# Kernel optimization log

Hardware: AMD Instinct MI355X
Metric: run time of the kernel (lower is better)

The kernel has to match this reference:

```python
import jax, jax.numpy as jnp
import numpy as np

HID = 10
IN_DIM = 256
B, H, W = 8, 96, 96


def _conv(x, w, b=None, pad=0):
    y = jax.lax.conv_general_dilated(x, w, (1, 1), [(pad, pad), (pad, pad)],
                                     dimension_numbers=('NCHW', 'OIHW', 'NCHW'))
    return y if b is None else y + b[None, :, None, None]


def _bn(x, g, b):
    # eval-mode InPlaceABN(Sync) with identity running stats -> per-channel affine
    return x * g[None, :, None, None] + b[None, :, None, None]


def _branch(x, w1, g1, b1, w2, g2, b2):
    # Conv3x3 -> BN -> ReLU -> Conv1x1 -> BN -> ReLU  (relation / comp_u / comp_l)
    y = jax.nn.relu(_bn(_conv(x, w1, pad=1), g1, b1))
    return jax.nn.relu(_bn(_conv(y, w2), g2, b2))


def _gru(x, h, gw, gb, cw, cg, cb):
    # ConvGRU with 1x1 kernels
    gates = _conv(jnp.concatenate([x, h], axis=1), gw, gb)
    r = jax.nn.sigmoid(gates[:, 0:1])
    u = jax.nn.sigmoid(gates[:, 1:2])
    cnm = jax.nn.relu(_bn(_conv(jnp.concatenate([x, r * h], axis=1), cw), cg, cb))
    return (1.0 - u) * h + u * cnm


def setup_inputs():
    key = jax.random.key(0)
    ks = iter(jax.random.split(key, 48))

    def nrm(shape, s=0.05):
        return jax.random.normal(next(ks), shape, jnp.float32) * s

    inp = {
        'f_nodes': jax.random.normal(next(ks), (2, B, HID, H, W), jnp.float32),
        'h_nodes': jax.random.normal(next(ks), (3, B, HID, H, W), jnp.float32),
        'p_nodes': jax.random.normal(next(ks), (7, B, HID, H, W), jnp.float32),
        'xh': jax.random.normal(next(ks), (B, IN_DIM, H, W), jnp.float32),
        'f_atts': jax.random.uniform(next(ks), (2, B, 1, H, W), jnp.float32),
        'p_atts': jax.random.uniform(next(ks), (7, B, 1, H, W), jnp.float32),
        # Decomposition.decomp_att: Conv3x3(257->256)+BN+ReLU, Conv1x1(256->2)+bias
        'da_w1': nrm((IN_DIM, IN_DIM + 1, 3, 3)),
        'da_g1': jnp.ones((IN_DIM,), jnp.float32),
        'da_b1': jnp.zeros((IN_DIM,), jnp.float32),
        'da_w2': nrm((2, IN_DIM, 1, 1)),
        'da_b2': jnp.zeros((2,), jnp.float32),
    }
    # relation (shared across children), comp_u, comp_l: Conv3x3(20->10)+BN+ReLU, Conv1x1(10->10)+BN+ReLU
    for p in ('rel', 'cu', 'cl'):
        inp[p + '_w1'] = nrm((HID, 2 * HID, 3, 3))
        inp[p + '_g1'] = jnp.ones((HID,), jnp.float32)
        inp[p + '_b1'] = jnp.zeros((HID,), jnp.float32)
        inp[p + '_w2'] = nrm((HID, HID, 1, 1))
        inp[p + '_g2'] = jnp.ones((HID,), jnp.float32)
        inp[p + '_b2'] = jnp.zeros((HID,), jnp.float32)
    # 3 ConvGRUs (cls_h), 1x1 kernels, stacked on leading dim
    inp['gru_gw'] = nrm((3, 2, 2 * HID, 1, 1))
    inp['gru_gb'] = jnp.zeros((3, 2), jnp.float32)
    inp['gru_cw'] = nrm((3, HID, 2 * HID, 1, 1))
    inp['gru_cg'] = jnp.ones((3, HID), jnp.float32)
    inp['gru_cb'] = jnp.zeros((3, HID), jnp.float32)
    return inp


def reference(f_nodes, h_nodes, p_nodes, xh, f_atts, p_atts,
              da_w1, da_g1, da_b1, da_w2, da_b2,
              rel_w1, rel_g1, rel_b1, rel_w2, rel_g2, rel_b2,
              cu_w1, cu_g1, cu_b1, cu_w2, cu_g2, cu_b2,
              cl_w1, cl_g1, cl_b1, cl_w2, cl_g2, cl_b2,
              gru_gw, gru_gb, gru_cw, gru_cg, gru_cb):
    parent, parent_att = f_nodes[1], f_atts[1]
    # Decomposition of full-body node into 2 half nodes
    dm = _conv(jnp.concatenate([parent_att, xh], axis=1), da_w1, pad=1)
    dm = jax.nn.relu(_bn(dm, da_g1, da_b1))
    dm = _conv(dm, da_w2, da_b2)  # [B, 2, H, W] decomposition map
    datt = jax.nn.softmax(dm, axis=1)
    decomp = [_branch(jnp.concatenate([parent * datt[:, i:i + 1] * parent_att,
                                       h_nodes[1 + i]], axis=1),
                      rel_w1, rel_g1, rel_b1, rel_w2, rel_g2, rel_b2)
              for i in range(2)]
    # node 0: background
    n0 = _gru(f_nodes[0] + p_nodes[0], h_nodes[0],
              gru_gw[0], gru_gb[0], gru_cw[0], gru_cg[0], gru_cb[0])
    # node 1: upper half = composition(upper parts 1-4) + decomposition
    up = jnp.sum(p_nodes[1:5], axis=0) * jnp.sum(p_atts[1:5], axis=0)
    comp_u = _branch(jnp.concatenate([h_nodes[1], up], axis=1),
                     cu_w1, cu_g1, cu_b1, cu_w2, cu_g2, cu_b2)
    n1 = _gru(comp_u + decomp[0], h_nodes[1],
              gru_gw[1], gru_gb[1], gru_cw[1], gru_cg[1], gru_cb[1])
    # node 2: lower half = composition(lower parts 5-6) + decomposition
    lo = jnp.sum(p_nodes[5:7], axis=0) * jnp.sum(p_atts[5:7], axis=0)
    comp_l = _branch(jnp.concatenate([h_nodes[2], lo], axis=1),
                     cl_w1, cl_g1, cl_b1, cl_w2, cl_g2, cl_b2)
    n2 = _gru(comp_l + decomp[1], h_nodes[2],
              gru_gw[2], gru_gb[2], gru_cw[2], gru_cg[2], gru_cb[2])
    return (jnp.stack([n0, n1, n2]), dm)
```

## Files before the change

kernel.cpp:

```cpp
#include <hip/hip_runtime.h>
#include <cstddef>
#include <cstdint>

constexpr int Bn    = 8;
constexpr int Hn    = 96;
constexpr int Wn    = 96;
constexpr int HWn   = Hn * Wn;
constexpr int BHWn  = Bn * HWn;
constexpr int B10HW = Bn * 10 * HWn;

using short8  = __attribute__((ext_vector_type(8))) short;
using ushort8 = __attribute__((ext_vector_type(8))) unsigned short;
using float4v = __attribute__((ext_vector_type(4))) float;

__device__ __forceinline__ unsigned short f2bf(float f) {
    unsigned u = __builtin_bit_cast(unsigned, f);
    u += 0x7FFFu + ((u >> 16) & 1u);
    return (unsigned short)(u >> 16);
}

__global__ void k_packw(const float* __restrict__ w1, short* __restrict__ wpk)
{
    const int o = blockIdx.x * 256 + threadIdx.x;
    if (o >= 663552) return;
    const int j    = o & 7;
    const int lane = (o >> 3) & 63;
    const int q    = (o >> 9) & 15;
    const int t    = o >> 13;
    const int co   = q * 16 + (lane & 15);
    const int ci   = (t / 9) * 32 + ((lane >> 4) & 3) * 8 + j;
    const int tap  = t % 9;
    const float f  = (ci < 257) ? w1[((size_t)co * 257 + ci) * 9 + tap] : 0.f;
    wpk[o] = (short)f2bf(f);
}

__global__ __launch_bounds__(256, 3)
void k_bigconv3(const float* __restrict__ xh, const float* __restrict__ patt,
                const short* __restrict__ wpk, const float* __restrict__ g1,
                const float* __restrict__ b1, const float* __restrict__ w2,
                const float* __restrict__ db2,
                float* __restrict__ dm_out, float* __restrict__ s01)
{
    __shared__ __align__(16) short xs[2][4][137][8];
    __shared__ float part[4][64][2];

    const int tid  = threadIdx.x;
    const int lane = tid & 63;
    const int wid  = tid >> 6;
    const int bx   = blockIdx.x;
    const int b    = bx & 7;
    const int r2   = bx >> 3;
    const int wseg = r2 % 3;
    const int hb   = r2 / 3;
    const int h0   = hb * 2, w0 = wseg * 32;
    const int am   = lane & 15;
    const int aq   = lane >> 4;

    float4v acc[4][4];
    #pragma unroll
    for (int i = 0; i < 4; ++i)
        #pragma unroll
        for (int j = 0; j < 4; ++j)
            acc[i][j] = float4v{0.f, 0.f, 0.f, 0.f};

    int arow[4], acol[4];
    #pragma unroll
    for (int mt = 0; mt < 4; ++mt) {
        const int m = mt * 16 + am;
        arow[mt] = m >> 5;
        acol[mt] = m & 31;
    }

    auto stageX = [&](int cb, int buf) {
        const int cig0 = cb * 32 + wid * 8;
        for (int pos = lane; pos < 136; pos += 64) {
            const int row = pos / 34, col = pos % 34;
            const int hh = h0 - 1 + row, ww = w0 - 1 + col;
            const bool inb = ((unsigned)hh < (unsigned)Hn) & ((unsigned)ww < (unsigned)Wn);
            const int off = hh * Wn + ww;
            ushort8 v;
            #pragma unroll
            for (int j = 0; j < 8; ++j) {
                const int ci = cig0 + j;
                float f = 0.f;
                if (inb && ci < 257)
                    f = (ci == 0) ? patt[b * HWn + off]
                                  : xh[((size_t)b * 256 + (ci - 1)) * HWn + off];
                v[j] = f2bf(f);
            }
            *(ushort8*)&xs[buf][wid][pos][0] = v;
        }
    };

    const short8* wp = (const short8*)wpk;
    const int qb = wid * 4;

    stageX(0, 0);
    short8 bfr[4], bnx[4];
    #pragma unroll
    for (int nt = 0; nt < 4; ++nt)
        bfr[nt] = wp[(size_t)(qb + nt) * 64 + lane];
    __syncthreads();

    for (int cb = 0; cb < 9; ++cb) {
        const int buf = cb & 1;
        for (int tap = 0; tap < 9; ++tap) {
            const int t = cb * 9 + tap;
            if (t < 80) {
                #pragma unroll
                for (int nt = 0; nt < 4; ++nt)
                    bnx[nt] = wp[((size_t)(t + 1) * 16 + qb + nt) * 64 + lane];
            }
            const int kh = tap / 3, kw = tap % 3;
            short8 afr[4];
            #pragma unroll
            for (int mt = 0; mt < 4; ++mt) {
                const int pos = (arow[mt] + kh) * 34 + (acol[mt] + kw);
                afr[mt] = *(const short8*)&xs[buf][aq][pos][0];
            }
            #pragma unroll
            for (int mt = 0; mt < 4; ++mt)
                #pragma unroll
                for (int nt = 0; nt < 4; ++nt)
                    acc[mt][nt] = __builtin_amdgcn_mfma_f32_16x16x32_bf16(
                        afr[mt], bfr[nt], acc[mt][nt], 0, 0, 0);
            #pragma unroll
            for (int nt = 0; nt < 4; ++nt) bfr[nt] = bnx[nt];
        }
        if (cb < 8) stageX(cb + 1, buf ^ 1);
        __syncthreads();
    }

    float gv[4], bv[4], wa[4], wbv[4];
    #pragma unroll
    for (int nt = 0; nt < 4; ++nt) {
        const int co = wid * 64 + nt * 16 + am;
        gv[nt]  = g1[co];
        bv[nt]  = b1[co];
        wa[nt]  = w2[co];
        wbv[nt] = w2[256 + co];
    }
    #pragma unroll
    for (int mt = 0; mt < 4; ++mt) {
        #pragma unroll
        for (int reg = 0; reg < 4; ++reg) {
            float s0 = 0.f, s1 = 0.f;
            #pragma unroll
            for (int nt = 0; nt < 4; ++nt) {
                const float y = fmaxf(fmaf(acc[mt][nt][reg], gv[nt], bv[nt]), 0.f);
                s0 = fmaf(wa[nt], y, s0);
                s1 = fmaf(wbv[nt], y, s1);
            }
            #pragma unroll
            for (int off = 1; off < 16; off <<= 1) {
                s0 += __shfl_xor(s0, off, 64);
                s1 += __shfl_xor(s1, off, 64);
            }
            if (am == 0) {
                const int m = mt * 16 + aq * 4 + reg;
                part[wid][m][0] = s0;
                part[wid][m][1] = s1;
            }
        }
    }
    __syncthreads();
    if (tid < 64) {
        const int m = tid, r = m >> 5, c = m & 31;
        const int off = (h0 + r) * Wn + (w0 + c);
        float d0 = part[0][m][0] + part[1][m][0] + part[2][m][0] + part[3][m][0] + db2[0];
        float d1 = part[0][m][1] + part[1][m][1] + part[2][m][1] + part[3][m][1] + db2[1];
        dm_out[(size_t)(b * 2) * HWn + off]     = d0;
        dm_out[(size_t)(b * 2 + 1) * HWn + off] = d1;
        const float mx = fmaxf(d0, d1);
        const float e0 = expf(d0 - mx), e1 = expf(d1 - mx);
        const float pa = patt[b * HWn + off];
        const float inv = pa / (e0 + e1);
        s01[b * HWn + off]        = e0 * inv;
        s01[BHWn + b * HWn + off] = e1 * inv;
    }
}

struct BranchW  { const float *w1, *g1, *b1, *w2, *g2, *b2; };
struct BranchW3 { BranchW p[3]; };

__global__ __launch_bounds__(256)
void k_branch(BranchW3 P, const float* __restrict__ parent, const float* __restrict__ h_nodes,
              const float* __restrict__ s01, const float* __restrict__ pn,
              const float* __restrict__ pa, float* __restrict__ bout)
{
    const int z  = blockIdx.y;
    const int pi = (z < 2) ? 0 : (z - 1);
    __shared__ float xt[20][10][34];
    __shared__ float paSum[340];
    __shared__ __align__(16) float wlt[9 * 20 * 12];
    __shared__ float w2l[100], g1l[10], b1l[10], g2l[10], b2l[10];

    const BranchW& Pw = P.p[pi];
    const int tid = threadIdx.x;
    for (int idx = tid; idx < 2160; idx += 256) {
        const int co = idx % 12, rem = idx / 12, ci = rem % 20, tap = rem / 20;
        wlt[idx] = (co < 10) ? Pw.w1[(co * 20 + ci) * 9 + tap] : 0.f;
    }
    if (tid < 100) w2l[tid] = Pw.w2[tid];
    if (tid < 10) {
        g1l[tid] = Pw.g1[tid]; b1l[tid] = Pw.b1[tid];
        g2l[tid] = Pw.g2[tid]; b2l[tid] = Pw.b2[tid];
    }

    const int bx = blockIdx.x;
    const int tw = bx % 3, th = (bx / 3) % 12, b = bx / 36;
    const int h0 = th * 8, w0 = tw * 32;

    const float* Ab;
    const float* sc = nullptr;
    const float* Bb = nullptr;
    int k0 = 0, k1 = -1;
    if (z == 0)      { Ab = parent; sc = s01;        Bb = h_nodes + (size_t)1 * B10HW; }
    else if (z == 1) { Ab = parent; sc = s01 + BHWn; Bb = h_nodes + (size_t)2 * B10HW; }
    else if (z == 2) { Ab = h_nodes + (size_t)1 * B10HW; k0 = 1; k1 = 4; }
    else             { Ab = h_nodes + (size_t)2 * B10HW; k0 = 5; k1 = 6; }

    if (z >= 2) {
        for (int idx = tid; idx < 340; idx += 256) {
            const int col = idx % 34, row = idx / 34;
            const int hh = h0 - 1 + row, ww = w0 - 1 + col;
            float s = 0.f;
            if (((unsigned)hh < (unsigned)Hn) & ((unsigned)ww < (unsigned)Wn)) {
                const int off = hh * Wn + ww;
                for (int k = k0; k <= k1; ++k)
                    s += pa[(size_t)(k * Bn + b) * HWn + off];
            }
            paSum[idx] = s;
        }
    }
    __syncthreads();

    for (int idx = tid; idx < 6800; idx += 256) {
        const int col = idx % 34, rem = idx / 34, row = rem % 10, ch = rem / 10;
        const int hh = h0 - 1 + row, ww = w0 - 1 + col;
        float v = 0.f;
        if (((unsigned)hh < (unsigned)Hn) & ((unsigned)ww < (unsigned)Wn)) {
            const int off = hh * Wn + ww;
            if (ch < 10) {
                v = Ab[((size_t)b * 10 + ch) * HWn + off];
                if (sc) v *= sc[b * HWn + off];
            } else if (z < 2) {
                v = Bb[((size_t)b * 10 + (ch - 10)) * HWn + off];
            } else {
                float s = 0.f;
                for (int k = k0; k <= k1; ++k)
                    s += pn[((size_t)(k * Bn + b) * 10 + (ch - 10)) * HWn + off];
                v = s * paSum[row * 34 + col];
            }
        }
        ((float*)xt)[idx] = v;
    }
    __syncthreads();

    const int r = tid >> 5, c = tid & 31;
    float a0 = 0, a1 = 0, a2 = 0, a3 = 0, a4 = 0, a5 = 0, a6 = 0, a7 = 0, a8 = 0, a9 = 0;
    #pragma unroll
    for (int tap = 0; tap < 9; ++tap) {
        const int kh = tap / 3, kw = tap % 3;
        #pragma unroll
        for (int ci = 0; ci < 20; ++ci) {
            const float xv = xt[ci][r + kh][c + kw];
            const float4 wA = *(const float4*)&wlt[(tap * 20 + ci) * 12];
            const float4 wB = *(const float4*)&wlt[(tap * 20 + ci) * 12 + 4];
            const float2 wC = *(const float2*)&wlt[(tap * 20 + ci) * 12 + 8];
            a0 = fmaf(wA.x, xv, a0); a1 = fmaf(wA.y, xv, a1);
            a2 = fmaf(wA.z, xv, a2); a3 = fmaf(wA.w, xv, a3);
            a4 = fmaf(wB.x, xv, a4); a5 = fmaf(wB.y, xv, a5);
            a6 = fmaf(wB.z, xv, a6); a7 = fmaf(wB.w, xv, a7);
            a8 = fmaf(wC.x, xv, a8); a9 = fmaf(wC.y, xv, a9);
        }
    }
    float acc[10] = {a0, a1, a2, a3, a4, a5, a6, a7, a8, a9};
    float y[10];
    #pragma unroll
    for (int co = 0; co < 10; ++co)
        y[co] = fmaxf(fmaf(acc[co], g1l[co], b1l[co]), 0.f);
    const int hw = (h0 + r) * Wn + (w0 + c);
    #pragma unroll
    for (int co = 0; co < 10; ++co) {
        float s = 0.f;
        #pragma unroll
        for (int i = 0; i < 10; ++i) s = fmaf(w2l[co * 10 + i], y[i], s);
        s = fmaxf(fmaf(s, g2l[co], b2l[co]), 0.f);
        bout[(size_t)z * B10HW + ((size_t)b * 10 + co) * HWn + hw] = s;
    }
}

__global__ void k_gru(const float* __restrict__ f_nodes, const float* __restrict__ h_nodes,
                      const float* __restrict__ p_nodes, const float* __restrict__ bout,
                      const float* __restrict__ gw, const float* __restrict__ gb,
                      const float* __restrict__ cw, const float* __restrict__ cg,
                      const float* __restrict__ cb, float* __restrict__ out)
{
    const int z = blockIdx.y;
    __shared__ float gwl[40], cwl[200], gbl[2], cgl[10], cbl[10];
    if (threadIdx.x < 40)  gwl[threadIdx.x] = gw[z * 40 + threadIdx.x];
    if (threadIdx.x < 200) cwl[threadIdx.x] = cw[z * 200 + threadIdx.x];
    if (threadIdx.x < 2)   gbl[threadIdx.x] = gb[z * 2 + threadIdx.x];
    if (threadIdx.x < 10) {
        cgl[threadIdx.x] = cg[z * 10 + threadIdx.x];
        cbl[threadIdx.x] = cb[z * 10 + threadIdx.x];
    }
    __syncthreads();

    const int p = blockIdx.x * 256 + threadIdx.x;
    const int b = p / HWn, hw = p % HWn;
    float x[10], h[10];
    #pragma unroll
    for (int c = 0; c < 10; ++c) {
        const size_t idx = ((size_t)b * 10 + c) * HWn + hw;
        if (z == 0)      x[c] = f_nodes[idx] + p_nodes[idx];
        else if (z == 1) x[c] = bout[(size_t)2 * B10HW + idx] + bout[idx];
        else             x[c] = bout[(size_t)3 * B10HW + idx] + bout[(size_t)1 * B10HW + idx];
        h[c] = h_nodes[(size_t)z * B10HW + idx];
    }
    float g0 = gbl[0], g1 = gbl[1];
    #pragma unroll
    for (int c = 0; c < 10; ++c) {
        g0 = fmaf(gwl[c],      x[c], g0);
        g0 = fmaf(gwl[10 + c], h[c], g0);
        g1 = fmaf(gwl[20 + c], x[c], g1);
        g1 = fmaf(gwl[30 + c], h[c], g1);
    }
    const float r = 1.f / (1.f + expf(-g0));
    const float u = 1.f / (1.f + expf(-g1));
    #pragma unroll
    for (int o = 0; o < 10; ++o) {
        float s = 0.f;
        #pragma unroll
        for (int c = 0; c < 10; ++c) {
            s = fmaf(cwl[o * 20 + c],      x[c],     s);
            s = fmaf(cwl[o * 20 + 10 + c], r * h[c], s);
        }
        s = fmaxf(fmaf(s, cgl[o], cbl[o]), 0.f);
        out[(size_t)z * B10HW + ((size_t)b * 10 + o) * HWn + hw] =
            (1.f - u) * h[o] + u * s;
    }
}

extern "C" void kernel_launch(void* const* d_in, const int* in_sizes, int n_in,
                              void* d_out, int out_size, void* d_ws, size_t ws_size,
                              hipStream_t stream)
{
    (void)in_sizes; (void)n_in; (void)out_size; (void)ws_size;

    const float* f_nodes = (const float*)d_in[0];
    const float* h_nodes = (const float*)d_in[1];
    const float* p_nodes = (const float*)d_in[2];
    const float* xh      = (const float*)d_in[3];
    const float* f_atts  = (const float*)d_in[4];
    const float* p_atts  = (const float*)d_in[5];
    const float* da_w1   = (const float*)d_in[6];
    const float* da_g1   = (const float*)d_in[7];
    const float* da_b1   = (const float*)d_in[8];
    const float* da_w2   = (const float*)d_in[9];
    const float* da_b2   = (const float*)d_in[10];

    BranchW3 P;
    for (int i = 0; i < 3; ++i) {
        P.p[i].w1 = (const float*)d_in[11 + 6 * i + 0];
        P.p[i].g1 = (const float*)d_in[11 + 6 * i + 1];
        P.p[i].b1 = (const float*)d_in[11 + 6 * i + 2];
        P.p[i].w2 = (const float*)d_in[11 + 6 * i + 3];
        P.p[i].g2 = (const float*)d_in[11 + 6 * i + 4];
        P.p[i].b2 = (const float*)d_in[11 + 6 * i + 5];
    }
    const float* gru_gw = (const float*)d_in[29];
    const float* gru_gb = (const float*)d_in[30];
    const float* gru_cw = (const float*)d_in[31];
    const float* gru_cg = (const float*)d_in[32];
    const float* gru_cb = (const float*)d_in[33];

    float* out    = (float*)d_out;
    float* dm_out = out + (size_t)3 * B10HW;

    float* ws     = (float*)d_ws;
    float* s01    = ws;
    float* bout   = s01 + 2 * BHWn;
    short* wpk    = (short*)bout;

    const float* patt   = f_atts + BHWn;
    const float* parent = f_nodes + B10HW;

    k_packw<<<dim3(2592), 256, 0, stream>>>(da_w1, wpk);
    k_bigconv3<<<dim3(1152), 256, 0, stream>>>(xh, patt, wpk, da_g1, da_b1,
                                               da_w2, da_b2, dm_out, s01);
    k_branch<<<dim3(288, 4), 256, 0, stream>>>(P, parent, h_nodes, s01,
                                               p_nodes, p_atts, bout);
    k_gru<<<dim3(288, 3), 256, 0, stream>>>(f_nodes, h_nodes, p_nodes, bout,
                                            gru_gw, gru_gb, gru_cw, gru_cg, gru_cb, out);
}
```

Measured before the change: 386.8 us.

## Pre-pack input to padded bf16 layout and async-stage tiles into LDS

Adds a pre-pass kernel that converts xh plus the attention channel into a zero-padded bf16 layout with 8 channels per 16-byte element. The big 3x3 conv then stages its input tiles with global_load_lds async copies, issued before the compute loop so the copy overlaps the MFMA work. This replaces the per-element fp32 loads, bounds checks and bf16 conversion that previously ran inside the conv. Branch conv weights are also pre-packed once in k_packw and read from global memory instead of being rebuilt in LDS by every block. The costs are an extra full pass over xh, a large workspace buffer, and a fallback path to the old conv kernel when the workspace is too small.

```diff
diff --git a/kernel.cpp b/kernel.cpp
--- a/kernel.cpp
+++ b/kernel.cpp
@@ -9,6 +9,12 @@
 constexpr int BHWn  = Bn * HWn;
 constexpr int B10HW = Bn * 10 * HWn;
 
+constexpr int XP_COLS        = 100;
+constexpr int XP_ROWS        = 100;
+constexpr int XP_PLANE       = XP_ROWS * XP_COLS;
+constexpr int XP_PLANE_BYTES = XP_PLANE * 16;
+constexpr int XP_OCT         = 36;
+
 using short8  = __attribute__((ext_vector_type(8))) short;
 using ushort8 = __attribute__((ext_vector_type(8))) unsigned short;
 using float4v = __attribute__((ext_vector_type(4))) float;
@@ -19,29 +25,73 @@
     return (unsigned short)(u >> 16);
 }
 
-__global__ void k_packw(const float* __restrict__ w1, short* __restrict__ wpk)
-{
-    const int o = blockIdx.x * 256 + threadIdx.x;
-    if (o >= 663552) return;
-    const int j    = o & 7;
-    const int lane = (o >> 3) & 63;
-    const int q    = (o >> 9) & 15;
-    const int t    = o >> 13;
-    const int co   = q * 16 + (lane & 15);
-    const int ci   = (t / 9) * 32 + ((lane >> 4) & 3) * 8 + j;
-    const int tap  = t % 9;
-    const float f  = (ci < 257) ? w1[((size_t)co * 257 + ci) * 9 + tap] : 0.f;
-    wpk[o] = (short)f2bf(f);
+__device__ __forceinline__ void async16(const void* g, void* l) {
+    auto gp = (__attribute__((address_space(1))) unsigned int*)(uintptr_t)g;
+    auto lp = (__attribute__((address_space(3))) unsigned int*)(unsigned)(uintptr_t)l;
+    __builtin_amdgcn_global_load_lds(gp, lp, 16, 0, 0);
+}
+
+struct BranchW  { const float *w1, *g1, *b1, *w2, *g2, *b2; };
+struct BranchW3 { BranchW p[3]; };
+
+__global__ void k_packw(const float* __restrict__ w1, short* __restrict__ wpk,
+                        BranchW3 P, float* __restrict__ wbk)
+{
+    if (blockIdx.x < 2592) {
+        const int o = blockIdx.x * 256 + threadIdx.x;
+        const int j    = o & 7;
+        const int lane = (o >> 3) & 63;
+        const int q    = (o >> 9) & 15;
+        const int t    = o >> 13;
+        const int co   = q * 16 + (lane & 15);
+        const int ci   = (t / 9) * 32 + ((lane >> 4) & 3) * 8 + j;
+        const int tap  = t % 9;
+        const float f  = (ci < 257) ? w1[((size_t)co * 257 + ci) * 9 + tap] : 0.f;
+        wpk[o] = (short)f2bf(f);
+    } else {
+        const int idx = (blockIdx.x - 2592) * 256 + threadIdx.x;
+        if (idx < 6480) {
+            const int pi = idx / 2160, r = idx % 2160;
+            const int co = r % 12, tci = r / 12;
+            const int tap = tci / 20, ci = tci % 20;
+            wbk[idx] = (co < 10) ? P.p[pi].w1[(co * 20 + ci) * 9 + tap] : 0.f;
+        }
+    }
+}
+
+__global__ void k_packx(const float* __restrict__ xh, const float* __restrict__ patt,
+                        ushort* __restrict__ xp)
+{
+    const int g  = blockIdx.x * 256 + threadIdx.x;
+    const int cw = g % XP_COLS;
+    int t = g / XP_COLS;
+    const int rh = t % XP_ROWS; t /= XP_ROWS;
+    const int o  = t % XP_OCT;
+    const int b  = t / XP_OCT;
+    const int hh = rh - 1, ww = cw - 1;
+    const bool inb = ((unsigned)hh < (unsigned)Hn) & ((unsigned)ww < (unsigned)Wn);
+    const int off = hh * Wn + ww;
+    ushort8 v;
+    #pragma unroll
+    for (int j = 0; j < 8; ++j) {
+        const int ci = o * 8 + j;
+        float f = 0.f;
+        if (inb && ci < 257)
+            f = (ci == 0) ? patt[b * HWn + off]
+                          : xh[((size_t)b * 256 + (ci - 1)) * HWn + off];
+        v[j] = f2bf(f);
+    }
+    *(ushort8*)&xp[(size_t)g * 8] = v;
 }
 
 __global__ __launch_bounds__(256, 3)
-void k_bigconv3(const float* __restrict__ xh, const float* __restrict__ patt,
+void k_bigconv3(const char* __restrict__ xp, const float* __restrict__ patt,
                 const short* __restrict__ wpk, const float* __restrict__ g1,
                 const float* __restrict__ b1, const float* __restrict__ w2,
                 const float* __restrict__ db2,
                 float* __restrict__ dm_out, float* __restrict__ s01)
 {
-    __shared__ __align__(16) short xs[2][4][137][8];
+    __shared__ __align__(16) short xs[2][4][194][8];
     __shared__ float part[4][64][2];
 
     const int tid  = threadIdx.x;
@@ -56,6 +106,15 @@
     const int am   = lane & 15;
     const int aq   = lane >> 4;
 
+    int poff[3];
+    #pragma unroll
+    for (int it = 0; it < 3; ++it) {
+        const int pos = it * 64 + lane;
+        const int row = pos / 34, col = pos - row * 34;
+        poff[it] = ((h0 + row) * XP_COLS + (w0 + col)) * 16;
+    }
+    const char* xpb = xp + ((size_t)b * XP_OCT + wid) * XP_PLANE_BYTES;
+
     float4v acc[4][4];
     #pragma unroll
     for (int i = 0; i < 4; ++i)
@@ -72,24 +131,10 @@
     }
 
     auto stageX = [&](int cb, int buf) {
-        const int cig0 = cb * 32 + wid * 8;
-        for (int pos = lane; pos < 136; pos += 64) {
-            const int row = pos / 34, col = pos % 34;
-            const int hh = h0 - 1 + row, ww = w0 - 1 + col;
-            const bool inb = ((unsigned)hh < (unsigned)Hn) & ((unsigned)ww < (unsigned)Wn);
-            const int off = hh * Wn + ww;
-            ushort8 v;
-            #pragma unroll
-            for (int j = 0; j < 8; ++j) {
-                const int ci = cig0 + j;
-                float f = 0.f;
-                if (inb && ci < 257)
-                    f = (ci == 0) ? patt[b * HWn + off]
-                                  : xh[((size_t)b * 256 + (ci - 1)) * HWn + off];
-                v[j] = f2bf(f);
-            }
-            *(ushort8*)&xs[buf][wid][pos][0] = v;
-        }
+        const char* src = xpb + (size_t)cb * (4 * XP_PLANE_BYTES);
+        #pragma unroll
+        for (int it = 0; it < 3; ++it)
+            async16(src + poff[it], &xs[buf][wid][it * 64][0]);
     };
 
     const short8* wp = (const short8*)wpk;
@@ -104,6 +149,7 @@
 
     for (int cb = 0; cb < 9; ++cb) {
         const int buf = cb & 1;
+        if (cb < 8) stageX(cb + 1, buf ^ 1);
         for (int tap = 0; tap < 9; ++tap) {
             const int t = cb * 9 + tap;
             if (t < 80) {
@@ -127,7 +173,6 @@
             #pragma unroll
             for (int nt = 0; nt < 4; ++nt) bfr[nt] = bnx[nt];
         }
-        if (cb < 8) stageX(cb + 1, buf ^ 1);
         __syncthreads();
     }
 
@@ -180,32 +225,166 @@
     }
 }
 
-struct BranchW  { const float *w1, *g1, *b1, *w2, *g2, *b2; };
-struct BranchW3 { BranchW p[3]; };
+__global__ __launch_bounds__(256, 3)
+void k_bigconv3_f(const float* __restrict__ xh, const float* __restrict__ patt,
+                  const short* __restrict__ wpk, const float* __restrict__ g1,
+                  const float* __restrict__ b1, const float* __restrict__ w2,
+                  const float* __restrict__ db2,
+                  float* __restrict__ dm_out, float* __restrict__ s01)
+{
+    __shared__ __align__(16) short xs[2][4][137][8];
+    __shared__ float part[4][64][2];
+
+    const int tid  = threadIdx.x;
+    const int lane = tid & 63;
+    const int wid  = tid >> 6;
+    const int bx   = blockIdx.x;
+    const int b    = bx & 7;
+    const int r2   = bx >> 3;
+    const int wseg = r2 % 3;
+    const int hb   = r2 / 3;
+    const int h0   = hb * 2, w0 = wseg * 32;
+    const int am   = lane & 15;
+    const int aq   = lane >> 4;
+
+    float4v acc[4][4];
+    #pragma unroll
+    for (int i = 0; i < 4; ++i)
+        #pragma unroll
+        for (int j = 0; j < 4; ++j)
+            acc[i][j] = float4v{0.f, 0.f, 0.f, 0.f};
+
+    int arow[4], acol[4];
+    #pragma unroll
+    for (int mt = 0; mt < 4; ++mt) {
+        const int m = mt * 16 + am;
+        arow[mt] = m >> 5;
+        acol[mt] = m & 31;
+    }
+
+    auto stageX = [&](int cb, int buf) {
+        const int cig0 = cb * 32 + wid * 8;
+        for (int pos = lane; pos < 136; pos += 64) {
+            const int row = pos / 34, col = pos % 34;
+            const int hh = h0 - 1 + row, ww = w0 - 1 + col;
+            const bool inb = ((unsigned)hh < (unsigned)Hn) & ((unsigned)ww < (unsigned)Wn);
+            const int off = hh * Wn + ww;
+            ushort8 v;
+            #pragma unroll
+            for (int j = 0; j < 8; ++j) {
+                const int ci = cig0 + j;
+                float f = 0.f;
+                if (inb && ci < 257)
+                    f = (ci == 0) ? patt[b * HWn + off]
+                                  : xh[((size_t)b * 256 + (ci - 1)) * HWn + off];
+                v[j] = f2bf(f);
+            }
+            *(ushort8*)&xs[buf][wid][pos][0] = v;
+        }
+    };
+
+    const short8* wp = (const short8*)wpk;
+    const int qb = wid * 4;
+
+    stageX(0, 0);
+    short8 bfr[4], bnx[4];
+    #pragma unroll
+    for (int nt = 0; nt < 4; ++nt)
+        bfr[nt] = wp[(size_t)(qb + nt) * 64 + lane];
+    __syncthreads();
+
+    for (int cb = 0; cb < 9; ++cb) {
+        const int buf = cb & 1;
+        for (int tap = 0; tap < 9; ++tap) {
+            const int t = cb * 9 + tap;
+            if (t < 80) {
+                #pragma unroll
+                for (int nt = 0; nt < 4; ++nt)
+                    bnx[nt] = wp[((size_t)(t + 1) * 16 + qb + nt) * 64 + lane];
+            }
+            const int kh = tap / 3, kw = tap % 3;
+            short8 afr[4];
+            #pragma unroll
+            for (int mt = 0; mt < 4; ++mt) {
+                const int pos = (arow[mt] + kh) * 34 + (acol[mt] + kw);
+                afr[mt] = *(const short8*)&xs[buf][aq][pos][0];
+            }
+            #pragma unroll
+            for (int mt = 0; mt < 4; ++mt)
+                #pragma unroll
+                for (int nt = 0; nt < 4; ++nt)
+                    acc[mt][nt] = __builtin_amdgcn_mfma_f32_16x16x32_bf16(
+                        afr[mt], bfr[nt], acc[mt][nt], 0, 0, 0);
+            #pragma unroll
+            for (int nt = 0; nt < 4; ++nt) bfr[nt] = bnx[nt];
+        }
+        if (cb < 8) stageX(cb + 1, buf ^ 1);
+        __syncthreads();
+    }
+
+    float gv[4], bv[4], wa[4], wbv[4];
+    #pragma unroll
+    for (int nt = 0; nt < 4; ++nt) {
+        const int co = wid * 64 + nt * 16 + am;
+        gv[nt]  = g1[co];
+        bv[nt]  = b1[co];
+        wa[nt]  = w2[co];
+        wbv[nt] = w2[256 + co];
+    }
+    #pragma unroll
+    for (int mt = 0; mt < 4; ++mt) {
+        #pragma unroll
+        for (int reg = 0; reg < 4; ++reg) {
+            float s0 = 0.f, s1 = 0.f;
+            #pragma unroll
+            for (int nt = 0; nt < 4; ++nt) {
+                const float y = fmaxf(fmaf(acc[mt][nt][reg], gv[nt], bv[nt]), 0.f);
+                s0 = fmaf(wa[nt], y, s0);
+                s1 = fmaf(wbv[nt], y, s1);
+            }
+            #pragma unroll
+            for (int off = 1; off < 16; off <<= 1) {
+                s0 += __shfl_xor(s0, off, 64);
+                s1 += __shfl_xor(s1, off, 64);
+            }
+            if (am == 0) {
+                const int m = mt * 16 + aq * 4 + reg;
+                part[wid][m][0] = s0;
+                part[wid][m][1] = s1;
+            }
+        }
+    }
+    __syncthreads();
+    if (tid < 64) {
+        const int m = tid, r = m >> 5, c = m & 31;
+        const int off = (h0 + r) * Wn + (w0 + c);
+        float d0 = part[0][m][0] + part[1][m][0] + part[2][m][0] + part[3][m][0] + db2[0];
+        float d1 = part[0][m][1] + part[1][m][1] + part[2][m][1] + part[3][m][1] + db2[1];
+        dm_out[(size_t)(b * 2) * HWn + off]     = d0;
+        dm_out[(size_t)(b * 2 + 1) * HWn + off] = d1;
+        const float mx = fmaxf(d0, d1);
+        const float e0 = expf(d0 - mx), e1 = expf(d1 - mx);
+        const float pa = patt[b * HWn + off];
+        const float inv = pa / (e0 + e1);
+        s01[b * HWn + off]        = e0 * inv;
+        s01[BHWn + b * HWn + off] = e1 * inv;
+    }
+}
 
 __global__ __launch_bounds__(256)
 void k_branch(BranchW3 P, const float* __restrict__ parent, const float* __restrict__ h_nodes,
               const float* __restrict__ s01, const float* __restrict__ pn,
-              const float* __restrict__ pa, float* __restrict__ bout)
+              const float* __restrict__ pa, const float* __restrict__ wbk,
+              float* __restrict__ bout)
 {
     const int z  = blockIdx.y;
     const int pi = (z < 2) ? 0 : (z - 1);
     __shared__ float xt[20][10][34];
     __shared__ float paSum[340];
-    __shared__ __align__(16) float wlt[9 * 20 * 12];
-    __shared__ float w2l[100], g1l[10], b1l[10], g2l[10], b2l[10];
 
     const BranchW& Pw = P.p[pi];
+    const float* __restrict__ wz = wbk + pi * 2160;
     const int tid = threadIdx.x;
-    for (int idx = tid; idx < 2160; idx += 256) {
-        const int co = idx % 12, rem = idx / 12, ci = rem % 20, tap = rem / 20;
-        wlt[idx] = (co < 10) ? Pw.w1[(co * 20 + ci) * 9 + tap] : 0.f;
-    }
-    if (tid < 100) w2l[tid] = Pw.w2[tid];
-    if (tid < 10) {
-        g1l[tid] = Pw.g1[tid]; b1l[tid] = Pw.b1[tid];
-        g2l[tid] = Pw.g2[tid]; b2l[tid] = Pw.b2[tid];
-    }
 
     const int bx = blockIdx.x;
     const int tw = bx % 3, th = (bx / 3) % 12, b = bx / 36;
@@ -258,35 +437,34 @@
     __syncthreads();
 
     const int r = tid >> 5, c = tid & 31;
-    float a0 = 0, a1 = 0, a2 = 0, a3 = 0, a4 = 0, a5 = 0, a6 = 0, a7 = 0, a8 = 0, a9 = 0;
+    float acc[10] = {0.f, 0.f, 0.f, 0.f, 0.f, 0.f, 0.f, 0.f, 0.f, 0.f};
     #pragma unroll
     for (int tap = 0; tap < 9; ++tap) {
         const int kh = tap / 3, kw = tap % 3;
         #pragma unroll
         for (int ci = 0; ci < 20; ++ci) {
             const float xv = xt[ci][r + kh][c + kw];
-            const float4 wA = *(const float4*)&wlt[(tap * 20 + ci) * 12];
-            const float4 wB = *(const float4*)&wlt[(tap * 20 + ci) * 12 + 4];
-            const float2 wC = *(const float2*)&wlt[(tap * 20 + ci) * 12 + 8];
-            a0 = fmaf(wA.x, xv, a0); a1 = fmaf(wA.y, xv, a1);
-            a2 = fmaf(wA.z, xv, a2); a3 = fmaf(wA.w, xv, a3);
-            a4 = fmaf(wB.x, xv, a4); a5 = fmaf(wB.y, xv, a5);
-            a6 = fmaf(wB.z, xv, a6); a7 = fmaf(wB.w, xv, a7);
-            a8 = fmaf(wC.x, xv, a8); a9 = fmaf(wC.y, xv, a9);
-        }
-    }
-    float acc[10] = {a0, a1, a2, a3, a4, a5, a6, a7, a8, a9};
+            const float4 wA = *(const float4*)(wz + (tap * 20 + ci) * 12);
+            const float4 wB = *(const float4*)(wz + (tap * 20 + ci) * 12 + 4);
+            const float2 wC = *(const float2*)(wz + (tap * 20 + ci) * 12 + 8);
+            acc[0] = fmaf(wA.x, xv, acc[0]); acc[1] = fmaf(wA.y, xv, acc[1]);
+            acc[2] = fmaf(wA.z, xv, acc[2]); acc[3] = fmaf(wA.w, xv, acc[3]);
+            acc[4] = fmaf(wB.x, xv, acc[4]); acc[5] = fmaf(wB.y, xv, acc[5]);
+            acc[6] = fmaf(wB.z, xv, acc[6]); acc[7] = fmaf(wB.w, xv, acc[7]);
+            acc[8] = fmaf(wC.x, xv, acc[8]); acc[9] = fmaf(wC.y, xv, acc[9]);
+        }
+    }
     float y[10];
     #pragma unroll
     for (int co = 0; co < 10; ++co)
-        y[co] = fmaxf(fmaf(acc[co], g1l[co], b1l[co]), 0.f);
+        y[co] = fmaxf(fmaf(acc[co], Pw.g1[co], Pw.b1[co]), 0.f);
     const int hw = (h0 + r) * Wn + (w0 + c);
     #pragma unroll
     for (int co = 0; co < 10; ++co) {
         float s = 0.f;
         #pragma unroll
-        for (int i = 0; i < 10; ++i) s = fmaf(w2l[co * 10 + i], y[i], s);
-        s = fmaxf(fmaf(s, g2l[co], b2l[co]), 0.f);
+        for (int i = 0; i < 10; ++i) s = fmaf(Pw.w2[co * 10 + i], y[i], s);
+        s = fmaxf(fmaf(s, Pw.g2[co], Pw.b2[co]), 0.f);
         bout[(size_t)z * B10HW + ((size_t)b * 10 + co) * HWn + hw] = s;
     }
 }
@@ -347,7 +525,7 @@
                               void* d_out, int out_size, void* d_ws, size_t ws_size,
                               hipStream_t stream)
 {
-    (void)in_sizes; (void)n_in; (void)out_size; (void)ws_size;
+    (void)in_sizes; (void)n_in; (void)out_size;
 
     const float* f_nodes = (const float*)d_in[0];
     const float* h_nodes = (const float*)d_in[1];
@@ -379,19 +557,30 @@
     float* out    = (float*)d_out;
     float* dm_out = out + (size_t)3 * B10HW;
 
-    float* ws     = (float*)d_ws;
-    float* s01    = ws;
-    float* bout   = s01 + 2 * BHWn;
-    short* wpk    = (short*)bout;
+    float* ws   = (float*)d_ws;
+    float* s01  = ws;
+    float* bout = s01 + 2 * BHWn;
+    short* wpk  = (short*)bout;
+    float* wbk  = bout + 4 * (size_t)B10HW;
+    const size_t XP_OFF_B = ((size_t)(2 * BHWn) + 4 * (size_t)B10HW + 6480) * 4;
+    char*  xp   = (char*)d_ws + XP_OFF_B;
+    const size_t WS_NEED = XP_OFF_B + (size_t)Bn * XP_OCT * XP_PLANE_BYTES;
+    const bool use_packed = ws_size >= WS_NEED;
 
     const float* patt   = f_atts + BHWn;
     const float* parent = f_nodes + B10HW;
 
-    k_packw<<<dim3(2592), 256, 0, stream>>>(da_w1, wpk);
-    k_bigconv3<<<dim3(1152), 256, 0, stream>>>(xh, patt, wpk, da_g1, da_b1,
-                                               da_w2, da_b2, dm_out, s01);
+    k_packw<<<dim3(2618), 256, 0, stream>>>(da_w1, wpk, P, wbk);
+    if (use_packed) {
+        k_packx<<<dim3(11250), 256, 0, stream>>>(xh, patt, (ushort*)xp);
+        k_bigconv3<<<dim3(1152), 256, 0, stream>>>(xp, patt, wpk, da_g1, da_b1,
+                                                   da_w2, da_b2, dm_out, s01);
+    } else {
+        k_bigconv3_f<<<dim3(1152), 256, 0, stream>>>(xh, patt, wpk, da_g1, da_b1,
+                                                     da_w2, da_b2, dm_out, s01);
+    }
     k_branch<<<dim3(288, 4), 256, 0, stream>>>(P, parent, h_nodes, s01,
-                                               p_nodes, p_atts, bout);
+                                               p_nodes, p_atts, wbk, bout);
     k_gru<<<dim3(288, 3), 256, 0, stream>>>(f_nodes, h_nodes, p_nodes, bout,
                                             gru_gw, gru_gb, gru_cw, gru_cg, gru_cb, out);
 }
```

Measured after the change: 393.2 us. Within noise of the previous version (+1.6%).
